# Optimization experiments

Hardware: AMD Instinct MI355X
Metric: run time of the kernel (lower is better)

## Reference

```python
import jax, jax.numpy as jnp
import numpy as np

N_CHANNEL = 64
N_BAND = 5
N_CLASS = 2
B = 64
K = 2 * N_CHANNEL  # nodes covered by the fully-connected edge_index


def _w(key, shape):
    fan_in = shape[0] if len(shape) == 2 else int(np.prod(shape[1:]))
    return (jax.random.normal(key, shape, jnp.float32) / np.float32(np.sqrt(fan_in)))


def setup_inputs() -> dict:
    key = jax.random.key(0)
    ks = jax.random.split(key, 22)
    d = {}
    d['x1'] = jax.random.normal(ks[0], (B, K, N_BAND), jnp.float32)
    d['x2'] = jax.random.normal(ks[1], (B, K, K), jnp.float32)
    # GCNConv params (weights stored (in, out); PyG applies linear then aggregates, bias after)
    d['gcn1_w'] = _w(ks[2], (N_BAND, 2 * N_BAND))
    d['gcn1_b'] = 0.01 * jax.random.normal(ks[3], (2 * N_BAND,), jnp.float32)
    d['gcn2_w'] = _w(ks[4], (2 * N_BAND, 1))
    d['gcn2_b'] = 0.01 * jax.random.normal(ks[5], (1,), jnp.float32)
    d['fcg_w'] = _w(ks[6], (K, K))
    d['fcg_b'] = 0.01 * jax.random.normal(ks[7], (K,), jnp.float32)
    d['conv1_w'] = _w(ks[8], (16, 1, 3, 3))   # OIHW
    d['conv1_b'] = 0.01 * jax.random.normal(ks[9], (16,), jnp.float32)
    d['conv2_w'] = _w(ks[10], (16, 16, 3, 3))
    d['conv2_b'] = 0.01 * jax.random.normal(ks[11], (16,), jnp.float32)
    d['fcc_w'] = _w(ks[12], (16 * K * K, K))
    d['fcc_b'] = 0.01 * jax.random.normal(ks[13], (K,), jnp.float32)
    d['fc1_w'] = _w(ks[14], (4 * N_CHANNEL, 2 * N_CHANNEL))
    d['fc1_b'] = 0.01 * jax.random.normal(ks[15], (2 * N_CHANNEL,), jnp.float32)
    d['fc2_w'] = _w(ks[16], (2 * N_CHANNEL, N_CHANNEL))
    d['fc2_b'] = 0.01 * jax.random.normal(ks[17], (N_CHANNEL,), jnp.float32)
    d['fc3_w'] = _w(ks[18], (N_CHANNEL, N_CLASS))
    d['fc3_b'] = 0.01 * jax.random.normal(ks[19], (N_CLASS,), jnp.float32)
    return d


def _gcn(x, W, b):
    # Faithful to original: edge_index is fully connected over the FIRST K rows only.
    # With default self-loops, normalized adjacency over rows [0,K) is (1/K)*ones(K,K)
    # (all degrees = K); every other row has only its self-loop (degree 1 -> identity).
    y = x @ W                                   # (B*N, out)
    y = y.at[:K].set(jnp.mean(y[:K], axis=0))   # broadcast mean over first K rows
    return y + b


def _conv(x, w, b):
    y = jax.lax.conv_general_dilated(x, w, (1, 1), 'SAME',
                                     dimension_numbers=('NCHW', 'OIHW', 'NCHW'))
    return jax.nn.relu(y + b[None, :, None, None])


def reference(x1, x2, gcn1_w, gcn1_b, gcn2_w, gcn2_b, fcg_w, fcg_b,
              conv1_w, conv1_b, conv2_w, conv2_b, fcc_w, fcc_b,
              fc1_w, fc1_b, fc2_w, fc2_b, fc3_w, fc3_b):
    Bn, N, Feat = x1.shape
    # GNN branch (dropout is identity in eval mode)
    h = x1.reshape(Bn * N, Feat)
    h = jax.nn.relu(_gcn(h, gcn1_w, gcn1_b))
    h = jax.nn.relu(_gcn(h, gcn2_w, gcn2_b))
    h = h.reshape(Bn, -1)                       # (B, 2*n_channel)
    g = jax.nn.relu(h @ fcg_w + fcg_b)
    # CNN branch
    c = x2[:, None]                             # (B,1,H,W)
    c = _conv(c, conv1_w, conv1_b)
    c = _conv(c, conv2_w, conv2_b)
    c = c.reshape(Bn, -1)                       # channel-major flatten, same as torch .view
    c = jax.nn.relu(c @ fcc_w + fcc_b)
    # Fusion MLP
    x = jnp.concatenate([c, g], axis=1)
    x = jax.nn.relu(x @ fc1_w + fc1_b)
    x = jax.nn.relu(x @ fc2_w + fc2_b)
    return jax.nn.sigmoid(x @ fc3_w + fc3_b)
```

## Files before the change

### kernel.cpp

```cpp
#include <hip/hip_runtime.h>
#include <hip/hip_bf16.h>


#define IMG     16384
#define FCC_K   262144
#define FCC_BLOCKS 512
#define FCC_KRANGE 512
#define FCC_CHUNK 64

typedef __attribute__((ext_vector_type(8))) short bf16x8;
typedef __attribute__((ext_vector_type(4))) float f32x4;
typedef __attribute__((ext_vector_type(4))) unsigned short us4;
typedef __attribute__((ext_vector_type(8))) unsigned short us8;

__device__ __forceinline__ unsigned short f2bf(float f) {
    unsigned u = __float_as_uint(f);
    unsigned r = (u + 0x7FFFu + ((u >> 16) & 1u)) >> 16;
    return (unsigned short)r;
}
__device__ __forceinline__ float bf2f(unsigned short b) {
    unsigned u = ((unsigned)b) << 16;
    return __uint_as_float(u);
}

__device__ __forceinline__ void sync_nodrain() {
    __builtin_amdgcn_sched_barrier(0);
    asm volatile("s_waitcnt lgkmcnt(0)" ::: "memory");
    __builtin_amdgcn_s_barrier();
    __builtin_amdgcn_sched_barrier(0);
}

__device__ __forceinline__ int fcc_swz64(int col, int k) {
    return col*64 + (k ^ ((((col >> 2) ^ col) & 7) << 3));
}

__global__ __launch_bounds__(256) void conv12_kernel(
    const float* __restrict__ x2,
    const float* __restrict__ w1,
    const float* __restrict__ b1,
    const float* __restrict__ w2,
    const float* __restrict__ b2,
    unsigned short* __restrict__ c2bf)
{
    __shared__ float sx2[8][130];
    __shared__ unsigned short sin[6*130*16];
    __shared__ unsigned short sB[5*512];
    __shared__ float sw1[144], sb1v[16];

    int tid = threadIdx.x;
    int blk = blockIdx.x;
    int b   = blk >> 5;
    int R0  = (blk & 31) * 4;

    if (tid < 144) sw1[tid] = w1[tid];
    if (tid < 16)  sb1v[tid] = b1[tid];

    for (int idx = tid; idx < 2560; idx += 256) {
        int q   = idx >> 9;
        int rem = idx & 511;
        int l   = rem >> 3;
        int e   = rem & 7;
        int k   = (l >> 4) * 8 + e;
        int oc  = l & 15;
        int ic  = k & 15;
        int dd  = 2*q + (k >> 4);
        unsigned short bits = 0;
        if (dd < 9) bits = f2bf(w2[oc*144 + ic*9 + dd]);
        sB[idx] = bits;
    }
    if (tid < 192) {
        int rr = tid >> 5, rem = tid & 31;
        int cc = (rem < 16) ? 0 : 129;
        sin[(rr*130 + cc)*16 + (rem & 15)] = 0;
    }
    {
        const float* xb = x2 + (size_t)b * IMG;
        for (int idx = tid; idx < 8*130; idx += 256) {
            int rr = idx / 130, cc = idx - rr*130;
            int ri = R0 - 2 + rr, gj = cc - 1;
            float v = 0.f;
            if (ri >= 0 && ri < 128 && gj >= 0 && gj < 128)
                v = xb[ri*128 + gj];
            sx2[rr][cc] = v;
        }
    }
    __syncthreads();

    for (int p = tid; p < 768; p += 256) {
        int rr = p >> 7;
        int cc = p & 127;
        int ri1 = R0 - 1 + rr;
        bool valid = (ri1 >= 0 && ri1 < 128);
        float in9[3][3];
        #pragma unroll
        for (int di = 0; di < 3; ++di)
          #pragma unroll
          for (int dj = 0; dj < 3; ++dj)
              in9[di][dj] = sx2[rr + di][cc + dj];
        us8 o0, o1;
        #pragma unroll
        for (int oc = 0; oc < 16; ++oc) {
            float acc = sb1v[oc];
            #pragma unroll
            for (int di = 0; di < 3; ++di)
              #pragma unroll
              for (int dj = 0; dj < 3; ++dj)
                  acc += in9[di][dj] * sw1[oc*9 + di*3 + dj];
            unsigned short bits = valid ? f2bf(fmaxf(acc, 0.f)) : (unsigned short)0;
            if (oc < 8) o0[oc] = bits; else o1[oc - 8] = bits;
        }
        unsigned short* dst = &sin[(rr*130 + cc + 1)*16];
        *reinterpret_cast<us8*>(dst)     = o0;
        *reinterpret_cast<us8*>(dst + 8) = o1;
    }
    __syncthreads();

    int lane = tid & 63;
    int wv   = tid >> 6;
    int ln   = lane & 15;
    int g    = lane >> 4;
    int ghalf = g & 1;

    int aoff[5];
    #pragma unroll
    for (int q = 0; q < 5; ++q) {
        int dd = 2*q + (g >> 1);
        if (dd > 8) dd = 8;
        int di = dd / 3, dj = dd % 3;
        aoff[q] = ((wv + di)*130 + ln + dj)*16 + ghalf*8;
    }

    bf16x8 bf[5];
    #pragma unroll
    for (int q = 0; q < 5; ++q)
        bf[q] = *reinterpret_cast<const bf16x8*>(&sB[q*512 + lane*8]);

    float bias_oc = b2[ln];
    int r = R0 + wv;
    unsigned short* outbase = c2bf + ((size_t)b*16 + ln)*IMG + r*128;

    #pragma unroll
    for (int t = 0; t < 8; ++t) {
        f32x4 acc = {0.f, 0.f, 0.f, 0.f};
        #pragma unroll
        for (int q = 0; q < 5; ++q) {
            bf16x8 a = *reinterpret_cast<const bf16x8*>(&sin[aoff[q] + t*256]);
            acc = __builtin_amdgcn_mfma_f32_16x16x32_bf16(a, bf[q], acc, 0, 0, 0);
        }
        int pc = t*16 + g*4;
        us4 pk;
        #pragma unroll
        for (int reg = 0; reg < 4; ++reg)
            pk[reg] = f2bf(fmaxf(acc[reg] + bias_oc, 0.f));
        *reinterpret_cast<us4*>(&outbase[pc]) = pk;
    }
}

#define STAGE_LOAD(ROWS, CI)                                                  \
    {                                                                         \
        const float* Wc_ = Wb + (size_t)(CI) * FCC_CHUNK * 128;               \
        _Pragma("unroll")                                                     \
        for (int r = 0; r < 8; ++r)                                           \
            ROWS[r] = *reinterpret_cast<const float4*>(                       \
                Wc_ + (size_t)(kO*8 + r)*128 + col0);                         \
    }

#define STAGE_WRITE(ROWS, BUF)                                                \
    {                                                                         \
        us8 vc0, vc1, vc2, vc3;                                               \
        _Pragma("unroll")                                                     \
        for (int r = 0; r < 8; ++r) {                                         \
            vc0[r] = f2bf(ROWS[r].x); vc1[r] = f2bf(ROWS[r].y);               \
            vc2[r] = f2bf(ROWS[r].z); vc3[r] = f2bf(ROWS[r].w);               \
        }                                                                     \
        *reinterpret_cast<us8*>(&(BUF)[fcc_swz64(col0+0, kO*8)]) = vc0;       \
        *reinterpret_cast<us8*>(&(BUF)[fcc_swz64(col0+1, kO*8)]) = vc1;       \
        *reinterpret_cast<us8*>(&(BUF)[fcc_swz64(col0+2, kO*8)]) = vc2;       \
        *reinterpret_cast<us8*>(&(BUF)[fcc_swz64(col0+3, kO*8)]) = vc3;       \
    }

#define COMPUTE_CHUNK(BUF, AF0, AF1)                                          \
    {                                                                         \
        _Pragma("unroll")                                                     \
        for (int j = 0; j < 8; ++j) {                                         \
            bf16x8 bfrag = *reinterpret_cast<const bf16x8*>(                  \
                &(BUF)[fcc_swz64(j*16 + ln, g*8)]);                           \
            acc[j] = __builtin_amdgcn_mfma_f32_16x16x32_bf16(AF0, bfrag, acc[j], 0, 0, 0); \
        }                                                                     \
        _Pragma("unroll")                                                     \
        for (int j = 0; j < 8; ++j) {                                         \
            bf16x8 bfrag = *reinterpret_cast<const bf16x8*>(                  \
                &(BUF)[fcc_swz64(j*16 + ln, 32 + g*8)]);                      \
            acc[j] = __builtin_amdgcn_mfma_f32_16x16x32_bf16(AF1, bfrag, acc[j], 0, 0, 0); \
        }                                                                     \
    }

__global__ __launch_bounds__(256, 2) void fcc_mfma(
    const unsigned short* __restrict__ c2bf,
    const float* __restrict__ W,
    unsigned short* __restrict__ partials)
{
    __shared__ unsigned short sWt[2][FCC_CHUNK*128];

    int tid  = threadIdx.x;
    int blk  = blockIdx.x;
    int k0   = blk * FCC_KRANGE;
    int lane = tid & 63, wv = tid >> 6;
    int ln   = lane & 15, g = lane >> 4;
    int q    = tid & 31;
    int kO   = tid >> 5;
    int col0 = q*4;

    f32x4 acc[8];
    #pragma unroll
    for (int j = 0; j < 8; ++j) acc[j] = (f32x4){0.f,0.f,0.f,0.f};

    const float* Wb = W + (size_t)k0 * 128;
    const unsigned short* arow = c2bf + (size_t)(16*wv + ln)*FCC_K + k0 + g*8;

    bf16x8 af[16];
    #pragma unroll
    for (int i = 0; i < 16; ++i)
        af[i] = *reinterpret_cast<const bf16x8*>(arow + i*32);

    float4 rows_a[8], rows_b[8];
    STAGE_LOAD(rows_a, 0)
    STAGE_LOAD(rows_b, 1)
    STAGE_WRITE(rows_a, sWt[0])
    sync_nodrain();

    #pragma unroll
    for (int d = 0; d < 4; ++d) {
        if (d < 3) STAGE_LOAD(rows_a, 2*d + 2)
        COMPUTE_CHUNK(sWt[0], af[4*d + 0], af[4*d + 1])
        sync_nodrain();
        STAGE_WRITE(rows_b, sWt[1])
        sync_nodrain();
        if (d < 3) STAGE_LOAD(rows_b, 2*d + 3)
        COMPUTE_CHUNK(sWt[1], af[4*d + 2], af[4*d + 3])
        sync_nodrain();
        if (d < 3) {
            STAGE_WRITE(rows_a, sWt[0])
            sync_nodrain();
        }
    }

    unsigned short* p = partials + (size_t)blk * 8192;
    #pragma unroll
    for (int j = 0; j < 8; ++j)
      #pragma unroll
      for (int reg = 0; reg < 4; ++reg) {
          int m = 16*wv + g*4 + reg;
          p[m*128 + j*16 + ln] = f2bf(acc[j][reg]);
      }
}

__global__ __launch_bounds__(512) void head_kernel(
    const unsigned short* __restrict__ partials,
    const float* __restrict__ fccb,
    const float* __restrict__ x1,
    const float* __restrict__ gW1, const float* __restrict__ gb1,
    const float* __restrict__ gW2, const float* __restrict__ gb2,
    const float* __restrict__ fcgW, const float* __restrict__ fcgb,
    const float* __restrict__ w1, const float* __restrict__ bb1,
    const float* __restrict__ w2, const float* __restrict__ bb2,
    const float* __restrict__ w3, const float* __restrict__ bb3,
    float* __restrict__ out)
{
    __shared__ float sred[4][128];
    __shared__ float sx[256], sh[128], s2[64], sh2[128];
    __shared__ float sW1[50], sb1s[10], sW2s[10], smean[10];
    __shared__ float sy1[128][10];
    int b = blockIdx.x, t = threadIdx.x;
    int o = t & 127, pr = t >> 7;

    {
        const unsigned short* pb = partials + (size_t)pr*8192 + (size_t)b*128 + o;
        float s = 0.f;
        #pragma unroll 8
        for (int p = 0; p < FCC_BLOCKS/4; ++p) s += bf2f(pb[(size_t)p*4*8192]);
        sred[pr][o] = s;
    }
    if (t < 50) sW1[t] = gW1[t];
    if (t >= 64 && t < 74) { sb1s[t-64] = gb1[t-64]; sW2s[t-64] = gW2[t-64]; }
    __syncthreads();

    if (t < 128)
        sx[t] = fmaxf(sred[0][t] + sred[1][t] + sred[2][t] + sred[3][t]
                      + fccb[t], 0.f);

    float y[10];
    if (t < 128) {
        int r = b*128 + t;
        float x[5];
        #pragma unroll
        for (int f = 0; f < 5; ++f) x[f] = x1[r*5 + f];
        #pragma unroll
        for (int oo = 0; oo < 10; ++oo) {
            float a = 0.f;
            #pragma unroll
            for (int f = 0; f < 5; ++f) a += x[f] * sW1[f*10 + oo];
            y[oo] = a;
        }
    }
    if (b == 0) {
        if (t < 128) {
            #pragma unroll
            for (int oo = 0; oo < 10; ++oo) sy1[t][oo] = y[oo];
        }
        __syncthreads();
        if (t < 10) {
            float s = 0.f;
            for (int rr = 0; rr < 128; ++rr) s += sy1[rr][t];
            smean[t] = fmaxf(s * (1.f/128.f) + sb1s[t], 0.f);
        }
        __syncthreads();
    }
    if (t < 128) {
        float h1row[10];
        if (b == 0) {
            #pragma unroll
            for (int oo = 0; oo < 10; ++oo) h1row[oo] = smean[oo];
        } else {
            #pragma unroll
            for (int oo = 0; oo < 10; ++oo) h1row[oo] = fmaxf(y[oo] + sb1s[oo], 0.f);
        }
        float y2 = 0.f;
        #pragma unroll
        for (int oo = 0; oo < 10; ++oo) y2 += h1row[oo] * sW2s[oo];
        sh2[t] = fmaxf(y2 + gb2[0], 0.f);
    }
    __syncthreads();

    if (t < 128) {
        float acc = fcgb[t];
        #pragma unroll 8
        for (int k = 0; k < 128; ++k) acc += sh2[k] * fcgW[k*128 + t];
        sx[128 + t] = fmaxf(acc, 0.f);
    }
    __syncthreads();

    if (t < 128) {
        float acc = bb1[t];
        for (int k = 0; k < 256; ++k) acc += sx[k] * w1[k*128 + t];
        sh[t] = fmaxf(acc, 0.f);
    }
    __syncthreads();
    if (t < 64) {
        float acc = bb2[t];
        for (int k = 0; k < 128; ++k) acc += sh[k] * w2[k*64 + t];
        s2[t] = fmaxf(acc, 0.f);
    }
    __syncthreads();
    if (t < 2) {
        float acc = bb3[t];
        for (int k = 0; k < 64; ++k) acc += s2[k] * w3[k*2 + t];
        out[b*2 + t] = 1.f / (1.f + __expf(-acc));
    }
}

extern "C" void kernel_launch(void* const* d_in, const int* in_sizes, int n_in,
                              void* d_out, int out_size, void* d_ws, size_t ws_size,
                              hipStream_t stream)
{
    const float* x1      = (const float*)d_in[0];
    const float* x2      = (const float*)d_in[1];
    const float* gcn1_w  = (const float*)d_in[2];
    const float* gcn1_b  = (const float*)d_in[3];
    const float* gcn2_w  = (const float*)d_in[4];
    const float* gcn2_b  = (const float*)d_in[5];
    const float* fcg_w   = (const float*)d_in[6];
    const float* fcg_b   = (const float*)d_in[7];
    const float* conv1_w = (const float*)d_in[8];
    const float* conv1_b = (const float*)d_in[9];
    const float* conv2_w = (const float*)d_in[10];
    const float* conv2_b = (const float*)d_in[11];
    const float* fcc_w   = (const float*)d_in[12];
    const float* fcc_b   = (const float*)d_in[13];
    const float* fc1_w   = (const float*)d_in[14];
    const float* fc1_b   = (const float*)d_in[15];
    const float* fc2_w   = (const float*)d_in[16];
    const float* fc2_b   = (const float*)d_in[17];
    const float* fc3_w   = (const float*)d_in[18];
    const float* fc3_b   = (const float*)d_in[19];
    float* out = (float*)d_out;

    unsigned short* c2bf     = (unsigned short*)d_ws;
    unsigned short* partials = c2bf + 16777216;

    conv12_kernel<<<2048, 256, 0, stream>>>(x2, conv1_w, conv1_b,
                                            conv2_w, conv2_b, c2bf);
    fcc_mfma<<<FCC_BLOCKS, 256, 0, stream>>>(c2bf, fcc_w, partials);
    head_kernel<<<64, 512, 0, stream>>>(partials, fcc_b,
                                        x1, gcn1_w, gcn1_b, gcn2_w, gcn2_b,
                                        fcg_w, fcg_b,
                                        fc1_w, fc1_b, fc2_w, fc2_b,
                                        fc3_w, fc3_b, out);
}
```

Baseline: 92.05 us.

## Stream fcc weights into LDS with async global_load_lds in a 4-deep ring

Swaps the register-staged fp32 weight loads followed by bf16 conversion and swizzled LDS writes for direct global-to-LDS async loads of raw fp32. A four-buffer ring of 32-row chunks is kept three chunks ahead, with vmcnt waits. Weights are converted to bf16 at read time from LDS using a cheaper round-half-up pack. This removes VGPR staging and LDS write traffic. In exchange, each MFMA fragment now needs eight scalar fp32 LDS reads, the LDS footprint doubles to 64KB, and the rounding differs slightly from round-to-nearest-even.

```diff
diff --git a/kernel.cpp b/kernel.cpp
--- a/kernel.cpp
+++ b/kernel.cpp
@@ -6,12 +6,17 @@
 #define FCC_K   262144
 #define FCC_BLOCKS 512
 #define FCC_KRANGE 512
-#define FCC_CHUNK 64
+#define CH_ROWS 32
+#define NCH 16
 
 typedef __attribute__((ext_vector_type(8))) short bf16x8;
 typedef __attribute__((ext_vector_type(4))) float f32x4;
 typedef __attribute__((ext_vector_type(4))) unsigned short us4;
 typedef __attribute__((ext_vector_type(8))) unsigned short us8;
+typedef __attribute__((ext_vector_type(4))) unsigned int u32x4;
+
+typedef __attribute__((address_space(3))) unsigned int lds_u32;
+typedef const __attribute__((address_space(1))) unsigned int glb_u32;
 
 __device__ __forceinline__ unsigned short f2bf(float f) {
     unsigned u = __float_as_uint(f);
@@ -21,6 +26,11 @@
 __device__ __forceinline__ float bf2f(unsigned short b) {
     unsigned u = ((unsigned)b) << 16;
     return __uint_as_float(u);
+}
+__device__ __forceinline__ unsigned pack2bf(float a, float b) {
+    unsigned ua = __float_as_uint(a) + 0x8000u;
+    unsigned ub = __float_as_uint(b) + 0x8000u;
+    return (ua >> 16) | (ub & 0xFFFF0000u);
 }
 
 __device__ __forceinline__ void sync_nodrain() {
@@ -28,10 +38,6 @@
     asm volatile("s_waitcnt lgkmcnt(0)" ::: "memory");
     __builtin_amdgcn_s_barrier();
     __builtin_amdgcn_sched_barrier(0);
-}
-
-__device__ __forceinline__ int fcc_swz64(int col, int k) {
-    return col*64 + (k ^ ((((col >> 2) ^ col) & 7) << 3));
 }
 
 __global__ __launch_bounds__(256) void conv12_kernel(
@@ -156,92 +162,80 @@
     }
 }
 
-#define STAGE_LOAD(ROWS, CI)                                                  \
-    {                                                                         \
-        const float* Wc_ = Wb + (size_t)(CI) * FCC_CHUNK * 128;               \
-        _Pragma("unroll")                                                     \
-        for (int r = 0; r < 8; ++r)                                           \
-            ROWS[r] = *reinterpret_cast<const float4*>(                       \
-                Wc_ + (size_t)(kO*8 + r)*128 + col0);                         \
-    }
-
-#define STAGE_WRITE(ROWS, BUF)                                                \
-    {                                                                         \
-        us8 vc0, vc1, vc2, vc3;                                               \
-        _Pragma("unroll")                                                     \
-        for (int r = 0; r < 8; ++r) {                                         \
-            vc0[r] = f2bf(ROWS[r].x); vc1[r] = f2bf(ROWS[r].y);               \
-            vc2[r] = f2bf(ROWS[r].z); vc3[r] = f2bf(ROWS[r].w);               \
-        }                                                                     \
-        *reinterpret_cast<us8*>(&(BUF)[fcc_swz64(col0+0, kO*8)]) = vc0;       \
-        *reinterpret_cast<us8*>(&(BUF)[fcc_swz64(col0+1, kO*8)]) = vc1;       \
-        *reinterpret_cast<us8*>(&(BUF)[fcc_swz64(col0+2, kO*8)]) = vc2;       \
-        *reinterpret_cast<us8*>(&(BUF)[fcc_swz64(col0+3, kO*8)]) = vc3;       \
-    }
-
-#define COMPUTE_CHUNK(BUF, AF0, AF1)                                          \
-    {                                                                         \
-        _Pragma("unroll")                                                     \
-        for (int j = 0; j < 8; ++j) {                                         \
-            bf16x8 bfrag = *reinterpret_cast<const bf16x8*>(                  \
-                &(BUF)[fcc_swz64(j*16 + ln, g*8)]);                           \
-            acc[j] = __builtin_amdgcn_mfma_f32_16x16x32_bf16(AF0, bfrag, acc[j], 0, 0, 0); \
-        }                                                                     \
-        _Pragma("unroll")                                                     \
-        for (int j = 0; j < 8; ++j) {                                         \
-            bf16x8 bfrag = *reinterpret_cast<const bf16x8*>(                  \
-                &(BUF)[fcc_swz64(j*16 + ln, 32 + g*8)]);                      \
-            acc[j] = __builtin_amdgcn_mfma_f32_16x16x32_bf16(AF1, bfrag, acc[j], 0, 0, 0); \
-        }                                                                     \
-    }
-
 __global__ __launch_bounds__(256, 2) void fcc_mfma(
     const unsigned short* __restrict__ c2bf,
     const float* __restrict__ W,
     unsigned short* __restrict__ partials)
 {
-    __shared__ unsigned short sWt[2][FCC_CHUNK*128];
+    __shared__ float sWf[4][CH_ROWS*128];
 
     int tid  = threadIdx.x;
     int blk  = blockIdx.x;
     int k0   = blk * FCC_KRANGE;
-    int lane = tid & 63, wv = tid >> 6;
+    int lane = tid & 63, wvid = tid >> 6;
     int ln   = lane & 15, g = lane >> 4;
-    int q    = tid & 31;
-    int kO   = tid >> 5;
-    int col0 = q*4;
 
     f32x4 acc[8];
     #pragma unroll
     for (int j = 0; j < 8; ++j) acc[j] = (f32x4){0.f,0.f,0.f,0.f};
 
     const float* Wb = W + (size_t)k0 * 128;
-    const unsigned short* arow = c2bf + (size_t)(16*wv + ln)*FCC_K + k0 + g*8;
+    const unsigned short* arow = c2bf + (size_t)(16*wvid + ln)*FCC_K + k0 + g*8;
 
     bf16x8 af[16];
     #pragma unroll
     for (int i = 0; i < 16; ++i)
         af[i] = *reinterpret_cast<const bf16x8*>(arow + i*32);
-
-    float4 rows_a[8], rows_b[8];
-    STAGE_LOAD(rows_a, 0)
-    STAGE_LOAD(rows_b, 1)
-    STAGE_WRITE(rows_a, sWt[0])
-    sync_nodrain();
-
-    #pragma unroll
-    for (int d = 0; d < 4; ++d) {
-        if (d < 3) STAGE_LOAD(rows_a, 2*d + 2)
-        COMPUTE_CHUNK(sWt[0], af[4*d + 0], af[4*d + 1])
+    __builtin_amdgcn_sched_barrier(0);
+
+    #pragma unroll
+    for (int c = 0; c < 3; ++c) {
+        const float* Wc = Wb + (size_t)c * CH_ROWS * 128;
+        float* buf = &sWf[c][0];
+        #pragma unroll
+        for (int i = 0; i < 4; ++i) {
+            int off = ((wvid*4 + i) << 8) + lane*4;
+            __builtin_amdgcn_global_load_lds((glb_u32*)(Wc + off),
+                                             (lds_u32*)(buf + off), 16, 0, 0);
+        }
+    }
+
+    #pragma unroll
+    for (int c = 0; c < NCH; ++c) {
+        if (c == NCH-2)      asm volatile("s_waitcnt vmcnt(4)" ::: "memory");
+        else if (c == NCH-1) asm volatile("s_waitcnt vmcnt(0)" ::: "memory");
+        else                 asm volatile("s_waitcnt vmcnt(8)" ::: "memory");
         sync_nodrain();
-        STAGE_WRITE(rows_b, sWt[1])
-        sync_nodrain();
-        if (d < 3) STAGE_LOAD(rows_b, 2*d + 3)
-        COMPUTE_CHUNK(sWt[1], af[4*d + 2], af[4*d + 3])
-        sync_nodrain();
-        if (d < 3) {
-            STAGE_WRITE(rows_a, sWt[0])
-            sync_nodrain();
+        if (c < NCH-3) {
+            const float* Wc = Wb + (size_t)(c+3) * CH_ROWS * 128;
+            float* buf = &sWf[(c+3) & 3][0];
+            #pragma unroll
+            for (int i = 0; i < 4; ++i) {
+                int off = ((wvid*4 + i) << 8) + lane*4;
+                __builtin_amdgcn_global_load_lds((glb_u32*)(Wc + off),
+                                                 (lds_u32*)(buf + off), 16, 0, 0);
+            }
+        }
+        const float* bufc = &sWf[c & 3][0];
+        bf16x8 afc = af[c];
+        #pragma unroll
+        for (int j = 0; j < 8; ++j) {
+            int cb = j*16 + ln;
+            float w0 = bufc[(g*8+0)*128 + cb];
+            float w1 = bufc[(g*8+1)*128 + cb];
+            float w2 = bufc[(g*8+2)*128 + cb];
+            float w3 = bufc[(g*8+3)*128 + cb];
+            float w4 = bufc[(g*8+4)*128 + cb];
+            float w5 = bufc[(g*8+5)*128 + cb];
+            float w6 = bufc[(g*8+6)*128 + cb];
+            float w7 = bufc[(g*8+7)*128 + cb];
+            u32x4 pk;
+            pk[0] = pack2bf(w0, w1);
+            pk[1] = pack2bf(w2, w3);
+            pk[2] = pack2bf(w4, w5);
+            pk[3] = pack2bf(w6, w7);
+            bf16x8 bfrag = *reinterpret_cast<bf16x8*>(&pk);
+            acc[j] = __builtin_amdgcn_mfma_f32_16x16x32_bf16(afc, bfrag, acc[j], 0, 0, 0);
         }
     }
 
@@ -250,7 +244,7 @@
     for (int j = 0; j < 8; ++j)
       #pragma unroll
       for (int reg = 0; reg < 4; ++reg) {
-          int m = 16*wv + g*4 + reg;
+          int m = 16*wvid + g*4 + reg;
           p[m*128 + j*16 + ln] = f2bf(acc[j][reg]);
       }
 }
```

Result: slower. 96.67 us (+5.0%).
